# Kernel optimization log

Measured on AMD Instinct MI355X. Metric: run time of the kernel, lower is better.

The kernel has to match this reference:

```python
import jax, jax.numpy as jnp
import numpy as np

B, H, O, DEPTH = 1024, 256, 32, 6  # batch, hidden(=latent), symbol vocab, full-binary-tree depth


def _lin(x, w, b):
    return x @ w.T + b


def _gru(x, h, wx, wh, bx, bh):
    # GRUAncestral / GRUFraternal cell: r,z,n gates, out = (1-z)*n + z*h
    r = jax.nn.sigmoid(_lin(x, wx[0], bx[0]) + _lin(h, wh[0], bh[0]))
    z = jax.nn.sigmoid(_lin(x, wx[1], bx[1]) + _lin(h, wh[1], bh[1]))
    n = jnp.tanh(_lin(x, wx[2], bx[2]) + r * _lin(h, wh[2], bh[2]))
    return (1.0 - z) * n + z * h


def setup_inputs() -> dict:
    key = jax.random.key(0)
    ks = jax.random.split(key, 16)
    def w(k, shape):
        fan_in = shape[-1]
        return jax.random.normal(k, shape, jnp.float32) * (1.0 / np.sqrt(fan_in))
    return {
        "z": jax.random.normal(ks[0], (B, 1, H), jnp.float32),
        "h2o_w": w(ks[1], (O, H)), "h2o_b": jnp.zeros((O,), jnp.float32),
        "w_c_w": w(ks[2], (H, H)), "w_c_b": jnp.zeros((H,), jnp.float32),
        "w_d_w": w(ks[3], (H, H)), "w_d_b": jnp.zeros((H,), jnp.float32),
        "z2h1_w": w(ks[4], (H, H)), "z2h1_b": jnp.zeros((H,), jnp.float32),
        "z2h2_w": w(ks[5], (H, H)), "z2h2_b": jnp.zeros((H,), jnp.float32),
        "gru_a_wx": w(ks[6], (3, H, O)), "gru_a_wh": w(ks[7], (3, H, H)),
        "gru_a_bx": jnp.zeros((3, H), jnp.float32), "gru_a_bh": jnp.zeros((3, H), jnp.float32),
        "gru_s_wx": w(ks[8], (3, H, O)), "gru_s_wh": w(ks[9], (3, H, H)),
        "gru_s_bx": jnp.zeros((3, H), jnp.float32), "gru_s_bh": jnp.zeros((3, H), jnp.float32),
        "depth": DEPTH,
    }


def reference(z, h2o_w, h2o_b, w_c_w, w_c_b, w_d_w, w_d_b,
              z2h1_w, z2h1_b, z2h2_w, z2h2_b,
              gru_a_wx, gru_a_wh, gru_a_bx, gru_a_bh,
              gru_s_wx, gru_s_wh, gru_s_bx, gru_s_bh,
              depth):
    preds = []  # preorder list of per-node predictions

    def rec(hidden_a, hidden, d):
        pred = _lin(hidden, h2o_w, h2o_b)          # [B,1,O]
        preds.append(pred)
        sp = jax.nn.softmax(pred, axis=2)
        if d > 1:
            # first child
            hf, spf = rec(_lin(hidden_a, w_c_w, w_c_b), _lin(hidden, w_d_w, w_d_b), d - 1)
            # second child: fraternal update on sibling state + ancestral update
            hf = _gru(spf, hf, gru_s_wx, gru_s_wh, gru_s_bx, gru_s_bh)
            hidden2 = hf + _gru(sp, hidden_a, gru_a_wx, gru_a_wh, gru_a_bx, gru_a_bh)
            rec(_lin(hidden_a, w_c_w, w_c_b), _lin(hidden2, w_d_w, w_d_b), d - 1)
        return hidden, sp

    rec(_lin(z, z2h1_w, z2h1_b), _lin(z, z2h2_w, z2h2_b), int(depth))
    return jnp.stack(preds)  # [2**depth-1, B, 1, O]
```

## Files before the change

### kernel.cpp

```cpp
#include <hip/hip_runtime.h>
#include <math.h>

#define Bdim 1024
#define DEPTHC 6

typedef __attribute__((ext_vector_type(8))) _Float16 f16x8;
typedef __attribute__((ext_vector_type(4))) float f32x4;

__device__ __forceinline__ unsigned short f2h(float x) {
    _Float16 h = (_Float16)x;
    unsigned short u;
    __builtin_memcpy(&u, &h, 2);
    return u;
}
__device__ __forceinline__ float h2f(unsigned short u) {
    _Float16 h;
    __builtin_memcpy(&h, &u, 2);
    return (float)h;
}
__device__ __forceinline__ float sigmf(float x) { return 1.0f / (1.0f + expf(-x)); }

__device__ __forceinline__ void glds16(const void* g, void* l) {
    __builtin_amdgcn_global_load_lds(
        (const __attribute__((address_space(1))) unsigned int*)g,
        (__attribute__((address_space(3))) unsigned int*)l, 16, 0, 0);
}

__device__ __forceinline__ void sbar() { asm volatile("s_barrier" ::: "memory"); }
template<int N> __device__ __forceinline__ void vmwait() {
    static_assert(N == 0 || N == 6 || N == 8 || N == 10, "unsupported vmcnt");
    if constexpr (N == 0)  asm volatile("s_waitcnt vmcnt(0)" ::: "memory");
    if constexpr (N == 6)  asm volatile("s_waitcnt vmcnt(6)" ::: "memory");
    if constexpr (N == 8)  asm volatile("s_waitcnt vmcnt(8)" ::: "memory");
    if constexpr (N == 10) asm volatile("s_waitcnt vmcnt(10)" ::: "memory");
    __builtin_amdgcn_sched_barrier(0);
}

__device__ __forceinline__ int preorder_idx(int level, int q) {
    int idx = 0, rem = DEPTHC;
    for (int k = level - 1; k >= 0; --k) {
        int b = (q >> k) & 1;
        idx += 1 + b * ((1 << (rem - 1)) - 1);
        rem--;
    }
    return idx;
}

struct CvtEnt { const float* src; unsigned short* dst; int n; int klog2; int pad; };
struct CvtArgs { CvtEnt e[8]; };

__global__ __launch_bounds__(256) void cvt_f16(CvtArgs a) {
    CvtEnt E = a.e[blockIdx.y];
    const int k = 1 << E.klog2;
    for (int t = blockIdx.x * 256 + threadIdx.x; t < E.n; t += gridDim.x * 256) {
        const float x = E.src[t];
        const int r = t >> E.klog2, c = t & (k - 1);
        if (!E.pad) {
            E.dst[(size_t)r * k + c] = f2h(x);
        } else {
            E.dst[(size_t)r * 2 * k + c] = f2h(x);
            E.dst[(size_t)r * 2 * k + k + c] = 0;
        }
    }
}

template<int BM>
__device__ __forceinline__ void gemm_body(
    int m0, int col0,
    const unsigned short* __restrict__ A2, const unsigned short* __restrict__ W2,
    const float* __restrict__ bias, float* __restrict__ Cf, int Nf,
    unsigned short* __restrict__ C2, int outStride, int outOffset,
    unsigned short* As, unsigned short* Ws)
{
    constexpr int MF = BM / 32;
    constexpr int AI = BM / 32;
    constexpr int ASZ = BM * 64;

    const int tid = threadIdx.x;
    const int w = tid >> 6, lane = tid & 63;
    const int p = m0 >> 10;
    const int wm = (w >> 1) * (BM / 2), wn = (w & 1) << 6;

    f32x4 acc[MF][4] = {};

    auto stage = [&](int buf, int s) {
        const int ka = s << 6;
        #pragma unroll
        for (int i = 0; i < AI; ++i) {
            const int r = w * (BM / 4) + (i << 3) + (lane >> 3);
            const int sl = (lane & 7) ^ (r & 7);
            glds16(A2 + (size_t)(m0 + r) * 256 + ka + (sl << 3),
                   &As[buf * ASZ + ((w * (BM / 4) + (i << 3)) << 6)]);
        }
        #pragma unroll
        for (int i = 0; i < 4; ++i) {
            const int r = (w << 5) + (i << 3) + (lane >> 3);
            const int sl = (lane & 7) ^ (r & 7);
            glds16(W2 + (size_t)(col0 + r) * 256 + ka + (sl << 3),
                   &Ws[buf * 8192 + (w << 11) + (i << 9)]);
        }
    };
    auto compute = [&](int buf) {
        #pragma unroll
        for (int kk = 0; kk < 2; ++kk) {
            f16x8 af[MF], bw[4];
            #pragma unroll
            for (int mf = 0; mf < MF; ++mf) {
                const int row = wm + (mf << 4) + (lane & 15);
                const int sl = (((kk << 2) | (lane >> 4)) ^ (row & 7)) << 3;
                af[mf] = *(const f16x8*)&As[buf * ASZ + (row << 6) + sl];
            }
            #pragma unroll
            for (int nf = 0; nf < 4; ++nf) {
                const int row = wn + (nf << 4) + (lane & 15);
                const int sl = (((kk << 2) | (lane >> 4)) ^ (row & 7)) << 3;
                bw[nf] = *(const f16x8*)&Ws[buf * 8192 + (row << 6) + sl];
            }
            __builtin_amdgcn_s_setprio(1);
            #pragma unroll
            for (int mf = 0; mf < MF; ++mf)
                #pragma unroll
                for (int nf = 0; nf < 4; ++nf)
                    acc[mf][nf] = __builtin_amdgcn_mfma_f32_16x16x32_f16(
                        af[mf], bw[nf], acc[mf][nf], 0, 0, 0);
            __builtin_amdgcn_s_setprio(0);
        }
    };

    stage(0, 0);
    #pragma unroll
    for (int s = 0; s < 4; ++s) {
        if (s + 1 < 4) { stage((s + 1) & 1, s + 1); vmwait<AI + 4>(); }
        else           { vmwait<0>(); }
        sbar();
        compute(s & 1);
        sbar();
    }

    const size_t oBase = (((size_t)(p * outStride + outOffset)) << 10) + (m0 & 1023);
    #pragma unroll
    for (int nf = 0; nf < 4; ++nf) {
        const int col = col0 + wn + (nf << 4) + (lane & 15);
        const float bj = bias[col];
        #pragma unroll
        for (int mf = 0; mf < MF; ++mf) {
            const int rb = wm + (mf << 4) + ((lane >> 4) << 2);
            #pragma unroll
            for (int r = 0; r < 4; ++r) {
                const float v = acc[mf][nf][r] + bj;
                const size_t orow = oBase + rb + r;
                if (Cf) Cf[orow * (size_t)Nf + col] = v;
                if (C2) C2[orow * 256 + col] = f2h(v);
            }
        }
    }
}

template<int BM>
__global__ __launch_bounds__(256) void mfma_gemm(
    const unsigned short* __restrict__ A2, const unsigned short* __restrict__ W2,
    const float* __restrict__ bias, float* __restrict__ Cf, int Nf,
    unsigned short* __restrict__ C2, int outStride, int outOffset)
{
    __shared__ __attribute__((aligned(16))) unsigned short As[2 * BM * 64];
    __shared__ __attribute__((aligned(16))) unsigned short Ws[2 * 8192];
    gemm_body<BM>(blockIdx.x * BM, blockIdx.y * 128, A2, W2, bias, Cf, Nf, C2,
                  outStride, outOffset, As, Ws);
}

struct GDesc {
    const unsigned short* A; const unsigned short* W; const float* bias;
    float* Cf; int Nf; unsigned short* C2; int outStride; int outOffset; int nbm;
};
struct GMulti { GDesc d[3]; int n0; int n01; };

template<int BM>
__global__ __launch_bounds__(256) void mfma_gemm_multi(GMulti g) {
    __shared__ __attribute__((aligned(16))) unsigned short As[2 * BM * 64];
    __shared__ __attribute__((aligned(16))) unsigned short Ws[2 * 8192];
    const int id = blockIdx.x;
    int di, base;
    if (id < g.n0)       { di = 0; base = 0; }
    else if (id < g.n01) { di = 1; base = g.n0; }
    else                 { di = 2; base = g.n01; }
    const GDesc D = g.d[di];
    const int lid = id - base;
    gemm_body<BM>((lid % D.nbm) * BM, (lid / D.nbm) * 128, D.A, D.W, D.bias,
                  D.Cf, D.Nf, D.C2, D.outStride, D.outOffset, As, Ws);
}

__global__ __launch_bounds__(256) void pred_grua(
    const unsigned short* __restrict__ H2, const float* __restrict__ h2o_w,
    const float* __restrict__ h2o_b, float* __restrict__ out,
    unsigned short* __restrict__ SP2, int level, int nodeStride, int nodeOffset,
    int npred,
    const unsigned short* __restrict__ SP2c, const float* __restrict__ GhA,
    const float* __restrict__ wx, const float* __restrict__ bx,
    const float* __restrict__ ha, unsigned short* __restrict__ ApfP)
{
    __shared__ float wsm[32][260];
    __shared__ float hsm[8][260];

    const int tid = threadIdx.x;

    if ((int)blockIdx.x < npred) {
        const int bid = blockIdx.x;
        const int p   = bid >> 7;
        const int b0  = (bid & 127) * 8;
        const int q   = p * nodeStride + nodeOffset;
        const unsigned short* Hrow = H2 + ((size_t)q * Bdim + b0) * 256;

        for (int t = tid * 4; t < 32 * 256; t += 1024) {
            const float4 v = *(const float4*)(h2o_w + t);
            const int j = t >> 8, k = t & 255;
            wsm[j][k] = v.x; wsm[j][k + 1] = v.y; wsm[j][k + 2] = v.z; wsm[j][k + 3] = v.w;
        }
        for (int t = tid * 4; t < 8 * 256; t += 1024) {
            const int r = t >> 8, k = t & 255;
            const ushort4 v4 = *(const ushort4*)(Hrow + (size_t)r * 256 + k);
            hsm[r][k + 0] = h2f(v4.x);
            hsm[r][k + 1] = h2f(v4.y);
            hsm[r][k + 2] = h2f(v4.z);
            hsm[r][k + 3] = h2f(v4.w);
        }
        __syncthreads();

        const int r = tid >> 5;
        const int j = tid & 31;
        float acc = 0.f;
        #pragma unroll 4
        for (int k = 0; k < 256; k += 4) {
            const float4 hv = *(const float4*)&hsm[r][k];
            const float4 wv = *(const float4*)&wsm[j][k];
            acc = fmaf(hv.x, wv.x, acc);
            acc = fmaf(hv.y, wv.y, acc);
            acc = fmaf(hv.z, wv.z, acc);
            acc = fmaf(hv.w, wv.w, acc);
        }
        acc += h2o_b[j];

        const int idx = preorder_idx(level, q);
        const int b   = b0 + r;
        out[((size_t)idx * Bdim + b) * 32 + j] = acc;

        float mx = acc;
        #pragma unroll
        for (int off = 16; off > 0; off >>= 1) mx = fmaxf(mx, __shfl_xor(mx, off, 32));
        const float e = expf(acc - mx);
        float sum = e;
        #pragma unroll
        for (int off = 16; off > 0; off >>= 1) sum += __shfl_xor(sum, off, 32);
        const float sp = e / sum;

        const size_t sbase = ((size_t)q * Bdim + b) * 64;
        SP2[sbase + j] = f2h(sp);
        SP2[sbase + 32 + j] = 0;
    } else {
        float (*sps)[33] = (float(*)[33])hsm;
        const int bid = blockIdx.x - npred;
        const int m0  = bid * 16;

        for (int t = tid; t < 16 * 32; t += 256) {
            const int r = t >> 5, k = t & 31;
            sps[r][k] = h2f(SP2c[((size_t)(m0 + r)) * 64 + k]);
        }
        __syncthreads();

        const int j = tid;
        float accr[16] = {}, accz[16] = {}, accn[16] = {};
        const float* wxj = wx + (size_t)j * 32;
        for (int k = 0; k < 32; ++k) {
            const float wr_ = wxj[k];
            const float wz_ = wxj[8192 + k];
            const float wn_ = wxj[16384 + k];
            #pragma unroll
            for (int r = 0; r < 16; ++r) {
                const float s = sps[r][k];
                accr[r] = fmaf(s, wr_, accr[r]);
                accz[r] = fmaf(s, wz_, accz[r]);
                accn[r] = fmaf(s, wn_, accn[r]);
            }
        }
        const float bxr = bx[j], bxz = bx[256 + j], bxn = bx[512 + j];
        float vals[16];
        #pragma unroll
        for (int r = 0; r < 16; ++r) {
            const int m = m0 + r;
            const int b = m & 1023;
            const float ghr = GhA[(size_t)b * 768 + j];
            const float ghz = GhA[(size_t)b * 768 + 256 + j];
            const float ghn = GhA[(size_t)b * 768 + 512 + j];
            const float rg = sigmf(accr[r] + bxr + ghr);
            const float zg = sigmf(accz[r] + bxz + ghz);
            const float ng = tanhf(accn[r] + bxn + rg * ghn);
            vals[r] = (1.f - zg) * ng + zg * ha[(size_t)b * 256 + j];
        }
        const size_t fb = ((size_t)(m0 >> 4) * 16 + (j >> 4)) * 256;
        #pragma unroll
        for (int g = 0; g < 4; ++g) {
            ushort4 st;
            st.x = f2h(vals[4 * g + 0]);
            st.y = f2h(vals[4 * g + 1]);
            st.z = f2h(vals[4 * g + 2]);
            st.w = f2h(vals[4 * g + 3]);
            *(ushort4*)(ApfP + fb + ((size_t)((j & 15) + (g << 4)) << 2)) = st;
        }
    }
}

template<int BM>
__global__ __launch_bounds__(256) void gru_s_fused(
    const unsigned short* __restrict__ Hn2, const unsigned short* __restrict__ SP2n,
    const unsigned short* __restrict__ gsW2, const unsigned short* __restrict__ gsX2,
    const float* __restrict__ gs_bx, const float* __restrict__ gs_bh,
    const unsigned short* __restrict__ ApfP, unsigned short* __restrict__ Ap2)
{
    constexpr int MF = BM / 32;
    constexpr int AI = BM / 32;
    constexpr int ASZ = BM * 64;
    __shared__ __attribute__((aligned(16))) unsigned short As[2 * ASZ];
    __shared__ __attribute__((aligned(16))) unsigned short Ws[2 * 12288];

    const int tid = threadIdx.x;
    const int w = tid >> 6, lane = tid & 63;
    const int col0 = blockIdx.y * 64;
    const int m0 = blockIdx.x * BM;
    const int p = m0 >> 10;
    const size_t aBase = (((size_t)(2 * p)) << 10) + (m0 & 1023);
    const int wr = w >> 1, wc = w & 1;
    const int sc = col0 >> 6;

    f32x4 a_sr[MF][2] = {}, a_sz[MF][2] = {}, a_snh[MF][2] = {}, a_snx[MF][2] = {};
    unsigned short hvv[MF][2][4];

    auto stage = [&](int buf, int s) {
        #pragma unroll
        for (int i = 0; i < AI; ++i) {
            const int r = w * (BM / 4) + (i << 3) + (lane >> 3);
            const int sl = (lane & 7) ^ (r & 7);
            const unsigned short* src;
            if (s < 4) src = Hn2 + (aBase + r) * 256 + (s << 6) + (sl << 3);
            else       src = SP2n + (aBase + r) * 64 + (sl << 3);
            glds16(src, &As[buf * ASZ + ((w * (BM / 4) + (i << 3)) << 6)]);
        }
        #pragma unroll
        for (int j = 0; j < 6; ++j) {
            const int R = w * 48 + (j << 3) + (lane >> 3);
            const int g = R >> 6, c = R & 63;
            const int sl = (lane & 7) ^ (R & 7);
            const size_t grow = (size_t)(g * 256 + col0 + c);
            const unsigned short* src;
            if (s < 4) src = gsW2 + grow * 256 + (s << 6) + (sl << 3);
            else       src = gsX2 + grow * 64 + (sl << 3);
            glds16(src, &Ws[buf * 12288 + ((w * 48 + (j << 3)) << 6)]);
        }
    };

    auto compute = [&](int buf, bool dohv, f32x4 (*tr)[2], f32x4 (*tz)[2], f32x4 (*tn)[2]) {
        if (dohv) {
            #pragma unroll
            for (int mf = 0; mf < MF; ++mf)
                #pragma unroll
                for (int nf = 0; nf < 2; ++nf)
                    #pragma unroll
                    for (int r = 0; r < 4; ++r) {
                        const int row = wr * (BM / 2) + (mf << 4) + ((lane >> 4) << 2) + r;
                        const int jcl = (wc << 5) + (nf << 4) + (lane & 15);
                        hvv[mf][nf][r] =
                            As[buf * ASZ + (row << 6) + (((jcl >> 3) ^ (row & 7)) << 3) + (jcl & 7)];
                    }
        }
        #pragma unroll
        for (int kk = 0; kk < 2; ++kk) {
            f16x8 af[MF], bw[3][2];
            #pragma unroll
            for (int mf = 0; mf < MF; ++mf) {
                const int row = wr * (BM / 2) + (mf << 4) + (lane & 15);
                const int sl = (((kk << 2) | (lane >> 4)) ^ (row & 7)) << 3;
                af[mf] = *(const f16x8*)&As[buf * ASZ + (row << 6) + sl];
            }
            #pragma unroll
            for (int g = 0; g < 3; ++g)
                #pragma unroll
                for (int nf = 0; nf < 2; ++nf) {
                    const int R = (g << 6) + (wc << 5) + (nf << 4) + (lane & 15);
                    const int sl = (((kk << 2) | (lane >> 4)) ^ (R & 7)) << 3;
                    bw[g][nf] = *(const f16x8*)&Ws[buf * 12288 + (R << 6) + sl];
                }
            __builtin_amdgcn_s_setprio(1);
            #pragma unroll
            for (int mf = 0; mf < MF; ++mf)
                #pragma unroll
                for (int nf = 0; nf < 2; ++nf) {
                    tr[mf][nf] = __builtin_amdgcn_mfma_f32_16x16x32_f16(af[mf], bw[0][nf], tr[mf][nf], 0, 0, 0);
                    tz[mf][nf] = __builtin_amdgcn_mfma_f32_16x16x32_f16(af[mf], bw[1][nf], tz[mf][nf], 0, 0, 0);
                    tn[mf][nf] = __builtin_amdgcn_mfma_f32_16x16x32_f16(af[mf], bw[2][nf], tn[mf][nf], 0, 0, 0);
                }
            __builtin_amdgcn_s_setprio(0);
        }
    };

    stage(0, 0);
    #pragma unroll
    for (int s = 0; s < 5; ++s) {
        if (s + 1 < 5) { stage((s + 1) & 1, s + 1); vmwait<AI + 6>(); }
        else           { vmwait<0>(); }
        sbar();
        if (s < 4) compute(s & 1, s == sc, a_sr, a_sz, a_snh);
        else       compute(s & 1, false, a_sr, a_sz, a_snx);
        sbar();
    }

    #pragma unroll
    for (int nf = 0; nf < 2; ++nf) {
        const int jc = col0 + (wc << 5) + (nf << 4) + (lane & 15);
        const int jt = (col0 >> 4) + (wc << 1) + nf;
        const float bsr  = gs_bx[jc] + gs_bh[jc];
        const float bsz  = gs_bx[256 + jc] + gs_bh[256 + jc];
        const float bsnx = gs_bx[512 + jc];
        const float bsnh = gs_bh[512 + jc];
        #pragma unroll
        for (int mf = 0; mf < MF; ++mf) {
            const int gmt = (m0 >> 4) + wr * (BM / 32) + mf;
            const ushort4 av = *(const ushort4*)(ApfP + ((size_t)gmt * 16 + jt) * 256 + (lane << 2));
            const unsigned short apv[4] = {av.x, av.y, av.z, av.w};
            #pragma unroll
            for (int r = 0; r < 4; ++r) {
                const int rowl = wr * (BM / 2) + (mf << 4) + ((lane >> 4) << 2) + r;
                const int m = m0 + rowl;
                const float rs = sigmf(a_sr[mf][nf][r] + bsr);
                const float zs = sigmf(a_sz[mf][nf][r] + bsz);
                const float ns = tanhf(a_snx[mf][nf][r] + bsnx + rs * (a_snh[mf][nf][r] + bsnh));
                const float hv = h2f(hvv[mf][nf][r]);
                const float val = (1.f - zs) * ns + zs * hv + h2f(apv[r]);
                Ap2[(size_t)m * 256 + jc] = f2h(val);
            }
        }
    }
}

extern "C" void kernel_launch(void* const* d_in, const int* in_sizes, int n_in,
                              void* d_out, int out_size, void* d_ws, size_t ws_size,
                              hipStream_t stream) {
    (void)in_sizes; (void)n_in; (void)out_size;

    const float* z      = (const float*)d_in[0];
    const float* h2o_w  = (const float*)d_in[1];
    const float* h2o_b  = (const float*)d_in[2];
    const float* w_c_w  = (const float*)d_in[3];
    const float* w_c_b  = (const float*)d_in[4];
    const float* w_d_w  = (const float*)d_in[5];
    const float* w_d_b  = (const float*)d_in[6];
    const float* z2h1_w = (const float*)d_in[7];
    const float* z2h1_b = (const float*)d_in[8];
    const float* z2h2_w = (const float*)d_in[9];
    const float* z2h2_b = (const float*)d_in[10];
    const float* ga_wx  = (const float*)d_in[11];
    const float* ga_wh  = (const float*)d_in[12];
    const float* ga_bx  = (const float*)d_in[13];
    const float* ga_bh  = (const float*)d_in[14];
    const float* gs_wx  = (const float*)d_in[15];
    const float* gs_wh  = (const float*)d_in[16];
    const float* gs_bx  = (const float*)d_in[17];
    const float* gs_bh  = (const float*)d_in[18];

    float* out = (float*)d_out;

    size_t off = 0;
    auto alloc = [&](size_t bytes) -> void* {
        void* r = (char*)d_ws + off;
        off += (bytes + 255) & ~(size_t)255;
        return r;
    };
    unsigned short* H2a  = (unsigned short*)alloc(16ull * 1024 * 256 * 2);
    unsigned short* H2b  = (unsigned short*)alloc(32ull * 1024 * 256 * 2);
    unsigned short* SP2a = (unsigned short*)alloc(16ull * 1024 * 64 * 2);
    unsigned short* SP2b = (unsigned short*)alloc(32ull * 1024 * 64 * 2);
    float* hacF0 = (float*)alloc(1024ull * 256 * 4);
    float* hacF1 = (float*)alloc(1024ull * 256 * 4);
    unsigned short* hac20 = (unsigned short*)alloc(1024ull * 256 * 2);
    unsigned short* hac21 = (unsigned short*)alloc(1024ull * 256 * 2);
    float* GhA = (float*)alloc(1024ull * 768 * 4);
    unsigned short* ApfP = (unsigned short*)alloc(16ull * 1024 * 256 * 2);
    unsigned short* Ap2 = (unsigned short*)alloc(16ull * 1024 * 256 * 2);
    unsigned short* z2  = (unsigned short*)alloc(1024ull * 256 * 2);
    unsigned short* wd2 = (unsigned short*)alloc(256ull * 256 * 2);
    unsigned short* wc2 = (unsigned short*)alloc(256ull * 256 * 2);
    unsigned short* z12 = (unsigned short*)alloc(256ull * 256 * 2);
    unsigned short* z22 = (unsigned short*)alloc(256ull * 256 * 2);
    unsigned short* gaW2 = (unsigned short*)alloc(768ull * 256 * 2);
    unsigned short* gsW2 = (unsigned short*)alloc(768ull * 256 * 2);
    unsigned short* gsX2 = (unsigned short*)alloc(768ull * 64 * 2);
    if (off > ws_size) return;

    const dim3 blk(256);

    CvtArgs ca = {{
        { z,      z2,   1024 * 256, 8, 0 },
        { w_d_w,  wd2,  256 * 256,  8, 0 },
        { w_c_w,  wc2,  256 * 256,  8, 0 },
        { z2h1_w, z12,  256 * 256,  8, 0 },
        { z2h2_w, z22,  256 * 256,  8, 0 },
        { ga_wh,  gaW2, 768 * 256,  8, 0 },
        { gs_wh,  gsW2, 768 * 256,  8, 0 },
        { gs_wx,  gsX2, 768 * 32,   5, 1 },
    }};
    cvt_f16<<<dim3(64, 8), blk, 0, stream>>>(ca);

    {
        GMulti gi;
        gi.d[0] = { z2, z12, z2h1_b, hacF0, 256, hac20, 1, 0, 16 };
        gi.d[1] = { z2, z22, z2h2_b, nullptr, 0, H2a, 1, 0, 16 };
        gi.d[2] = gi.d[1];
        gi.n0 = 32; gi.n01 = 64;
        mfma_gemm_multi<64><<<dim3(64), blk, 0, stream>>>(gi);
    }
    pred_grua<<<dim3(128), blk, 0, stream>>>(H2a, h2o_w, h2o_b, out, SP2a, 0, 1, 0,
                                             128, nullptr, nullptr, nullptr, nullptr,
                                             nullptr, nullptr);

    unsigned short* cur2 = H2a;  unsigned short* nxt2 = H2b;
    unsigned short* spc  = SP2a; unsigned short* spn  = SP2b;
    float* hf = hacF0;  float* hn = hacF1;
    unsigned short* hf2 = hac20; unsigned short* hn2 = hac21;

    for (int l = 0; l < DEPTHC - 1; ++l) {
        const int M = (1 << l) * Bdim;
        const bool small = (M <= 8192);
        const int BMv = small ? 64 : 128;
        const int nbm = M / BMv;
        const int nbh = 1024 / BMv;

        {
            GMulti g1;
            g1.d[0] = { cur2, wd2, w_d_b, nullptr, 0, nxt2, 2, 0, nbm };
            g1.d[1] = { hf2, gaW2, ga_bh, GhA, 768, nullptr, 1, 0, nbh };
            g1.d[2] = { hf2, wc2, w_c_b, hn, 256, hn2, 1, 0, nbh };
            const int nb0 = nbm * 2, nb1 = nbh * 6;
            const int nb2 = (l < DEPTHC - 2) ? nbh * 2 : 0;
            g1.n0 = nb0; g1.n01 = nb0 + nb1;
            const int ntot = nb0 + nb1 + nb2;
            if (small) mfma_gemm_multi<64><<<dim3(ntot), blk, 0, stream>>>(g1);
            else       mfma_gemm_multi<128><<<dim3(ntot), blk, 0, stream>>>(g1);
        }
        pred_grua<<<dim3(M / 8 + M / 16), blk, 0, stream>>>(
            nxt2, h2o_w, h2o_b, out, spn, l + 1, 2, 0, M / 8,
            spc, GhA, ga_wx, ga_bx, hf, ApfP);
        if (small) gru_s_fused<64><<<dim3(M / 64, 4), blk, 0, stream>>>(nxt2, spn, gsW2, gsX2, gs_bx, gs_bh, ApfP, Ap2);
        else       gru_s_fused<128><<<dim3(M / 128, 4), blk, 0, stream>>>(nxt2, spn, gsW2, gsX2, gs_bx, gs_bh, ApfP, Ap2);
        if (small) mfma_gemm<64><<<dim3(M / 64, 2), blk, 0, stream>>>(Ap2, wd2, w_d_b, nullptr, 0, nxt2, 2, 1);
        else       mfma_gemm<128><<<dim3(M / 128, 2), blk, 0, stream>>>(Ap2, wd2, w_d_b, nullptr, 0, nxt2, 2, 1);
        pred_grua<<<dim3(M / 8), blk, 0, stream>>>(
            nxt2, h2o_w, h2o_b, out, spn, l + 1, 2, 1, M / 8,
            nullptr, nullptr, nullptr, nullptr, nullptr, nullptr);

        unsigned short* t2;
        t2 = cur2; cur2 = nxt2; nxt2 = t2;
        t2 = spc;  spc  = spn;  spn  = t2;
        float* tf = hf; hf = hn; hn = tf;
        t2 = hf2; hf2 = hn2; hn2 = t2;
    }
}
```

Measured before the change: 491.9 us.

## Compute h2o prediction with MFMA on fp16 weights with LDS-staged tiles

Replaces the scalar FP32 dot-product prediction path (8 rows per block, weights reloaded and converted per block) with an MFMA 16x16x32 f16 GEMM over 128-row tiles. It uses double-buffered global_load_lds staging with swizzled LDS and a pre-converted fp16 copy of h2o_w. Softmax is then done from the accumulator fragments with 16-lane shuffles. This cuts per-block weight reloading and scalar FMA cost, but reduces block count by 16x for the prediction part, which may lower parallelism at small levels, and it adds fp16 rounding of the weights.

```diff
diff --git a/kernel.cpp b/kernel.cpp
--- a/kernel.cpp
+++ b/kernel.cpp
@@ -28,8 +28,9 @@
 
 __device__ __forceinline__ void sbar() { asm volatile("s_barrier" ::: "memory"); }
 template<int N> __device__ __forceinline__ void vmwait() {
-    static_assert(N == 0 || N == 6 || N == 8 || N == 10, "unsupported vmcnt");
+    static_assert(N == 0 || N == 4 || N == 6 || N == 8 || N == 10, "unsupported vmcnt");
     if constexpr (N == 0)  asm volatile("s_waitcnt vmcnt(0)" ::: "memory");
+    if constexpr (N == 4)  asm volatile("s_waitcnt vmcnt(4)" ::: "memory");
     if constexpr (N == 6)  asm volatile("s_waitcnt vmcnt(6)" ::: "memory");
     if constexpr (N == 8)  asm volatile("s_waitcnt vmcnt(8)" ::: "memory");
     if constexpr (N == 10) asm volatile("s_waitcnt vmcnt(10)" ::: "memory");
@@ -47,7 +48,7 @@
 }
 
 struct CvtEnt { const float* src; unsigned short* dst; int n; int klog2; int pad; };
-struct CvtArgs { CvtEnt e[8]; };
+struct CvtArgs { CvtEnt e[9]; };
 
 __global__ __launch_bounds__(256) void cvt_f16(CvtArgs a) {
     CvtEnt E = a.e[blockIdx.y];
@@ -189,8 +190,8 @@
                   D.Cf, D.Nf, D.C2, D.outStride, D.outOffset, As, Ws);
 }
 
-__global__ __launch_bounds__(256) void pred_grua(
-    const unsigned short* __restrict__ H2, const float* __restrict__ h2o_w,
+__global__ __launch_bounds__(256) void pred_mfma_grua(
+    const unsigned short* __restrict__ H2, const unsigned short* __restrict__ h2o2,
     const float* __restrict__ h2o_b, float* __restrict__ out,
     unsigned short* __restrict__ SP2, int level, int nodeStride, int nodeOffset,
     int npred,
@@ -198,65 +199,109 @@
     const float* __restrict__ wx, const float* __restrict__ bx,
     const float* __restrict__ ha, unsigned short* __restrict__ ApfP)
 {
-    __shared__ float wsm[32][260];
-    __shared__ float hsm[8][260];
+    __shared__ __attribute__((aligned(16))) unsigned short As[2 * 8192];
+    __shared__ __attribute__((aligned(16))) unsigned short Wsm[8192];
 
     const int tid = threadIdx.x;
+    const int w = tid >> 6, lane = tid & 63;
 
     if ((int)blockIdx.x < npred) {
-        const int bid = blockIdx.x;
-        const int p   = bid >> 7;
-        const int b0  = (bid & 127) * 8;
-        const int q   = p * nodeStride + nodeOffset;
-        const unsigned short* Hrow = H2 + ((size_t)q * Bdim + b0) * 256;
-
-        for (int t = tid * 4; t < 32 * 256; t += 1024) {
-            const float4 v = *(const float4*)(h2o_w + t);
-            const int j = t >> 8, k = t & 255;
-            wsm[j][k] = v.x; wsm[j][k + 1] = v.y; wsm[j][k + 2] = v.z; wsm[j][k + 3] = v.w;
-        }
-        for (int t = tid * 4; t < 8 * 256; t += 1024) {
-            const int r = t >> 8, k = t & 255;
-            const ushort4 v4 = *(const ushort4*)(Hrow + (size_t)r * 256 + k);
-            hsm[r][k + 0] = h2f(v4.x);
-            hsm[r][k + 1] = h2f(v4.y);
-            hsm[r][k + 2] = h2f(v4.z);
-            hsm[r][k + 3] = h2f(v4.w);
-        }
-        __syncthreads();
-
-        const int r = tid >> 5;
-        const int j = tid & 31;
-        float acc = 0.f;
-        #pragma unroll 4
-        for (int k = 0; k < 256; k += 4) {
-            const float4 hv = *(const float4*)&hsm[r][k];
-            const float4 wv = *(const float4*)&wsm[j][k];
-            acc = fmaf(hv.x, wv.x, acc);
-            acc = fmaf(hv.y, wv.y, acc);
-            acc = fmaf(hv.z, wv.z, acc);
-            acc = fmaf(hv.w, wv.w, acc);
-        }
-        acc += h2o_b[j];
+        const int m0g = blockIdx.x * 128;
+        const int p = m0g >> 10;
+        const int q = p * nodeStride + nodeOffset;
+        const int b0 = m0g & 1023;
+        const size_t aBase = ((size_t)q << 10) + b0;
+
+        #pragma unroll
+        for (int i = 0; i < 4; ++i) {
+            const int r = (i << 3) + (lane >> 3);
+            const int sl = (lane & 7) ^ (r & 7);
+            glds16(h2o2 + (size_t)r * 256 + (w << 6) + (sl << 3),
+                   &Wsm[(w << 11) + (i << 9)]);
+        }
+
+        auto stageA = [&](int buf, int s) {
+            #pragma unroll
+            for (int i = 0; i < 4; ++i) {
+                const int r = (w << 5) + (i << 3) + (lane >> 3);
+                const int sl = (lane & 7) ^ (r & 7);
+                glds16(H2 + (aBase + r) * 256 + (s << 6) + (sl << 3),
+                       &As[buf * 8192 + (((w << 5) + (i << 3)) << 6)]);
+            }
+        };
+
+        f32x4 acc[2][2] = {};
+
+        auto compute = [&](int buf, int s) {
+            #pragma unroll
+            for (int kk = 0; kk < 2; ++kk) {
+                f16x8 af[2], bw[2];
+                #pragma unroll
+                for (int mf = 0; mf < 2; ++mf) {
+                    const int row = (w << 5) + (mf << 4) + (lane & 15);
+                    const int sl = (((kk << 2) | (lane >> 4)) ^ (row & 7)) << 3;
+                    af[mf] = *(const f16x8*)&As[buf * 8192 + (row << 6) + sl];
+                }
+                #pragma unroll
+                for (int nf = 0; nf < 2; ++nf) {
+                    const int rowb = (nf << 4) + (lane & 15);
+                    const int sl = (((kk << 2) | (lane >> 4)) ^ (rowb & 7)) << 3;
+                    bw[nf] = *(const f16x8*)&Wsm[(s << 11) + (rowb << 6) + sl];
+                }
+                __builtin_amdgcn_s_setprio(1);
+                #pragma unroll
+                for (int mf = 0; mf < 2; ++mf)
+                    #pragma unroll
+                    for (int nf = 0; nf < 2; ++nf)
+                        acc[mf][nf] = __builtin_amdgcn_mfma_f32_16x16x32_f16(
+                            af[mf], bw[nf], acc[mf][nf], 0, 0, 0);
+                __builtin_amdgcn_s_setprio(0);
+            }
+        };
+
+        stageA(0, 0);
+        #pragma unroll
+        for (int s = 0; s < 4; ++s) {
+            if (s + 1 < 4) { stageA((s + 1) & 1, s + 1); vmwait<4>(); }
+            else           { vmwait<0>(); }
+            sbar();
+            compute(s & 1, s);
+            sbar();
+        }
 
         const int idx = preorder_idx(level, q);
-        const int b   = b0 + r;
-        out[((size_t)idx * Bdim + b) * 32 + j] = acc;
-
-        float mx = acc;
-        #pragma unroll
-        for (int off = 16; off > 0; off >>= 1) mx = fmaxf(mx, __shfl_xor(mx, off, 32));
-        const float e = expf(acc - mx);
-        float sum = e;
-        #pragma unroll
-        for (int off = 16; off > 0; off >>= 1) sum += __shfl_xor(sum, off, 32);
-        const float sp = e / sum;
-
-        const size_t sbase = ((size_t)q * Bdim + b) * 64;
-        SP2[sbase + j] = f2h(sp);
-        SP2[sbase + 32 + j] = 0;
+        const int colb = lane & 15;
+        const float bj0 = h2o_b[colb];
+        const float bj1 = h2o_b[16 + colb];
+
+        #pragma unroll
+        for (int mf = 0; mf < 2; ++mf) {
+            #pragma unroll
+            for (int r = 0; r < 4; ++r) {
+                const int rowl = (w << 5) + (mf << 4) + ((lane >> 4) << 2) + r;
+                const int b = b0 + rowl;
+                const float v0 = acc[mf][0][r] + bj0;
+                const float v1 = acc[mf][1][r] + bj1;
+                const size_t obase = (((size_t)idx << 10) + b) * 32;
+                out[obase + colb] = v0;
+                out[obase + 16 + colb] = v1;
+                float mx = fmaxf(v0, v1);
+                #pragma unroll
+                for (int off = 8; off > 0; off >>= 1) mx = fmaxf(mx, __shfl_xor(mx, off, 16));
+                const float e0 = expf(v0 - mx), e1 = expf(v1 - mx);
+                float sum = e0 + e1;
+                #pragma unroll
+                for (int off = 8; off > 0; off >>= 1) sum += __shfl_xor(sum, off, 16);
+                const float inv = 1.0f / sum;
+                const size_t sbase = (((size_t)q << 10) + b) * 64;
+                SP2[sbase + colb] = f2h(e0 * inv);
+                SP2[sbase + 16 + colb] = f2h(e1 * inv);
+                SP2[sbase + 32 + colb] = 0;
+                SP2[sbase + 48 + colb] = 0;
+            }
+        }
     } else {
-        float (*sps)[33] = (float(*)[33])hsm;
+        float (*sps)[33] = (float(*)[33])As;
         const int bid = blockIdx.x - npred;
         const int m0  = bid * 16;
 
@@ -491,6 +536,7 @@
     unsigned short* gaW2 = (unsigned short*)alloc(768ull * 256 * 2);
     unsigned short* gsW2 = (unsigned short*)alloc(768ull * 256 * 2);
     unsigned short* gsX2 = (unsigned short*)alloc(768ull * 64 * 2);
+    unsigned short* h2o2 = (unsigned short*)alloc(32ull * 256 * 2);
     if (off > ws_size) return;
 
     const dim3 blk(256);
@@ -504,8 +550,9 @@
         { ga_wh,  gaW2, 768 * 256,  8, 0 },
         { gs_wh,  gsW2, 768 * 256,  8, 0 },
         { gs_wx,  gsX2, 768 * 32,   5, 1 },
+        { h2o_w,  h2o2, 32 * 256,   8, 0 },
     }};
-    cvt_f16<<<dim3(64, 8), blk, 0, stream>>>(ca);
+    cvt_f16<<<dim3(64, 9), blk, 0, stream>>>(ca);
 
     {
         GMulti gi;
@@ -515,9 +562,9 @@
         gi.n0 = 32; gi.n01 = 64;
         mfma_gemm_multi<64><<<dim3(64), blk, 0, stream>>>(gi);
     }
-    pred_grua<<<dim3(128), blk, 0, stream>>>(H2a, h2o_w, h2o_b, out, SP2a, 0, 1, 0,
-                                             128, nullptr, nullptr, nullptr, nullptr,
-                                             nullptr, nullptr);
+    pred_mfma_grua<<<dim3(8), blk, 0, stream>>>(H2a, h2o2, h2o_b, out, SP2a, 0, 1, 0,
+                                                8, nullptr, nullptr, nullptr, nullptr,
+                                                nullptr, nullptr);
 
     unsigned short* cur2 = H2a;  unsigned short* nxt2 = H2b;
     unsigned short* spc  = SP2a; unsigned short* spn  = SP2b;
@@ -543,15 +590,15 @@
             if (small) mfma_gemm_multi<64><<<dim3(ntot), blk, 0, stream>>>(g1);
             else       mfma_gemm_multi<128><<<dim3(ntot), blk, 0, stream>>>(g1);
         }
-        pred_grua<<<dim3(M / 8 + M / 16), blk, 0, stream>>>(
-            nxt2, h2o_w, h2o_b, out, spn, l + 1, 2, 0, M / 8,
+        pred_mfma_grua<<<dim3(M / 128 + M / 16), blk, 0, stream>>>(
+            nxt2, h2o2, h2o_b, out, spn, l + 1, 2, 0, M / 128,
             spc, GhA, ga_wx, ga_bx, hf, ApfP);
         if (small) gru_s_fused<64><<<dim3(M / 64, 4), blk, 0, stream>>>(nxt2, spn, gsW2, gsX2, gs_bx, gs_bh, ApfP, Ap2);
         else       gru_s_fused<128><<<dim3(M / 128, 4), blk, 0, stream>>>(nxt2, spn, gsW2, gsX2, gs_bx, gs_bh, ApfP, Ap2);
         if (small) mfma_gemm<64><<<dim3(M / 64, 2), blk, 0, stream>>>(Ap2, wd2, w_d_b, nullptr, 0, nxt2, 2, 1);
         else       mfma_gemm<128><<<dim3(M / 128, 2), blk, 0, stream>>>(Ap2, wd2, w_d_b, nullptr, 0, nxt2, 2, 1);
-        pred_grua<<<dim3(M / 8), blk, 0, stream>>>(
-            nxt2, h2o_w, h2o_b, out, spn, l + 1, 2, 1, M / 8,
+        pred_mfma_grua<<<dim3(M / 128), blk, 0, stream>>>(
+            nxt2, h2o2, h2o_b, out, spn, l + 1, 2, 1, M / 128,
             nullptr, nullptr, nullptr, nullptr, nullptr, nullptr);
 
         unsigned short* t2;
```

After: 486.1 us. No clear change (-1.2%).
